# Performance work log

Hardware: AMD Instinct MI355X
Metric: run time of the kernel (lower is better)

The kernel has to match this reference:

```python
import jax, jax.numpy as jnp
import numpy as np

CH = 16        # channel_n
HID = 128      # hidden_size
IN_CH = 3      # input_channels (locked each step)
FIRE_RATE = 0.5


def _dwconv3x3(x, w, b):
    # depthwise 3x3, reflect padding (torch padding_mode='reflect', padding=1)
    xp = jnp.pad(x, ((0, 0), (0, 0), (1, 1), (1, 1)), mode='reflect')
    y = jax.lax.conv_general_dilated(
        xp, w, window_strides=(1, 1), padding='VALID',
        dimension_numbers=('NCHW', 'OIHW', 'NCHW'), feature_group_count=CH)
    return y + b[None, :, None, None]


def _conv1x1(x, w, b=None):
    # w: (out_ch, in_ch) -- squeezed 1x1 conv kernel
    y = jnp.einsum('bchw,oc->bohw', x, w)
    return y if b is None else y + b[None, :, None, None]


def setup_inputs() -> dict:
    key = jax.random.key(0)
    ks = jax.random.split(key, 8)
    B, H, W = 4, 256, 256
    x = jax.random.normal(ks[0], (B, CH, H, W), dtype=jnp.float32)
    # depthwise kernels: (CH, 1, 3, 3)
    p0_w = jax.random.normal(ks[1], (CH, 1, 3, 3), dtype=jnp.float32) * (1.0 / 3.0)
    p0_b = jax.random.normal(ks[2], (CH,), dtype=jnp.float32) * 0.1
    p1_w = jax.random.normal(ks[3], (CH, 1, 3, 3), dtype=jnp.float32) * (1.0 / 3.0)
    p1_b = jax.random.normal(ks[4], (CH,), dtype=jnp.float32) * 0.1
    # fc0: Conv2d(3*CH -> HID, k=1); fc1: Conv2d(HID -> CH, k=1, bias=False)
    fc0_w = jax.random.normal(ks[5], (HID, 3 * CH), dtype=jnp.float32) * (1.0 / np.sqrt(3 * CH))
    fc0_b = jax.random.normal(ks[6], (HID,), dtype=jnp.float32) * 0.1
    # NOTE: torch zero-inits fc1; we use small random weights so the reference is non-trivial.
    fc1_w = jax.random.normal(ks[7], (CH, HID), dtype=jnp.float32) * (0.1 / np.sqrt(HID))
    return {"x": x, "p0_w": p0_w, "p0_b": p0_b, "p1_w": p1_w, "p1_b": p1_b,
            "fc0_w": fc0_w, "fc0_b": fc0_b, "fc1_w": fc1_w, "steps": 32}


def reference(x, p0_w, p0_b, p1_w, p1_b, fc0_w, fc0_b, fc1_w, steps):
    B, _, H, W = x.shape
    input_image = x[:, :IN_CH]  # clone of input channels, re-written each step
    keys = jax.random.split(jax.random.key(42), steps)

    @jax.checkpoint
    def step(x, key):
        # perceive: depthwise 3x3 x2, concat with state
        z1 = _dwconv3x3(x, p0_w, p0_b)
        z2 = _dwconv3x3(x, p1_w, p1_b)
        y = jnp.concatenate([x, z1, z2], axis=1)        # [B, 3*CH, H, W]
        # 1x1-conv MLP
        dx = jax.nn.relu(_conv1x1(y, fc0_w, fc0_b))      # [B, HID, H, W]
        dx = _conv1x1(dx, fc1_w)                         # [B, CH, H, W]
        # stochastic fire mask: rand > fire_rate, broadcast over channels
        mask = (jax.random.uniform(key, (B, 1, H, W), dtype=x.dtype) > FIRE_RATE).astype(x.dtype)
        x = x + dx * mask                                # residual update
        x = x.at[:, :IN_CH].set(input_image)             # channel lock
        return x, None

    x, _ = jax.lax.scan(step, x, keys)
    out = x[:, 3]  # segmentation channel
    return out, x
```

## Files before the change

### kernel.cpp

```cpp
#include <hip/hip_runtime.h>
#include <cstdint>

#define CH     16
#define HPIX   256
#define WPIX   256
#define BATCH  4
#define HID    128
#define STEPS  32
#define PLANE  (HPIX * WPIX)
#define MASK_N (BATCH * PLANE)

#define TW 16
#define TH 8
#define XTW 18
#define XTH 10
#define NPX (XTH * XTW)
#define HSF 20

typedef _Float16 half8  __attribute__((ext_vector_type(8)));
typedef _Float16 half4e __attribute__((ext_vector_type(4)));
typedef float floatx4  __attribute__((ext_vector_type(4)));
typedef float floatx16 __attribute__((ext_vector_type(16)));

__host__ __device__ static inline void tf2x32(uint32_t k0, uint32_t k1,
                                              uint32_t x0, uint32_t x1,
                                              uint32_t& o0, uint32_t& o1) {
  const uint32_t ks2 = k0 ^ k1 ^ 0x1BD11BDAu;
#define TFROT(a) { x0 += x1; x1 = (x1 << (a)) | (x1 >> (32 - (a))); x1 ^= x0; }
  x0 += k0;  x1 += k1;
  TFROT(13) TFROT(15) TFROT(26) TFROT(6)
  x0 += k1;  x1 += ks2 + 1u;
  TFROT(17) TFROT(29) TFROT(16) TFROT(24)
  x0 += ks2; x1 += k0 + 2u;
  TFROT(13) TFROT(15) TFROT(26) TFROT(6)
  x0 += k0;  x1 += k1 + 3u;
  TFROT(17) TFROT(29) TFROT(16) TFROT(24)
  x0 += k1;  x1 += ks2 + 4u;
  TFROT(13) TFROT(15) TFROT(26) TFROT(6)
  x0 += ks2; x1 += k0 + 5u;
#undef TFROT
  o0 = x0; o1 = x1;
}

__global__ __launch_bounds__(256) void prep_weights(
    const float* __restrict__ fc0_w, const float* __restrict__ fc0_b,
    const float* __restrict__ fc1_w,
    const float* __restrict__ p0_w, const float* __restrict__ p0_b,
    const float* __restrict__ p1_w, const float* __restrict__ p1_b,
    _Float16* __restrict__ Mh, _Float16* __restrict__ W1h,
    float* __restrict__ bp) {
  const int idx = blockIdx.x * 256 + threadIdx.x;
  if (idx < 9 * HID * CH) {
    const int tap = idx / (HID * CH);
    const int rem = idx - tap * (HID * CH);
    const int h = rem >> 4, c = rem & 15;
    float m = fc0_w[h * 48 + 16 + c] * p0_w[c * 9 + tap]
            + fc0_w[h * 48 + 32 + c] * p1_w[c * 9 + tap];
    if (tap == 4) m += fc0_w[h * 48 + c];
    Mh[(tap * HID + h) * CH + c] = (_Float16)m;
  } else if (idx < 9 * HID * CH + CH * HID) {
    const int i2 = idx - 9 * HID * CH;
    W1h[i2] = (_Float16)fc1_w[i2];
  } else if (idx < 9 * HID * CH + CH * HID + HID) {
    const int h = idx - (9 * HID * CH + CH * HID);
    float s = fc0_b[h];
    for (int c = 0; c < CH; ++c)
      s += fc0_w[h * 48 + 16 + c] * p0_b[c]
         + fc0_w[h * 48 + 32 + c] * p1_b[c];
    bp[h] = s;
  }
}

__global__ __launch_bounds__(256) void nca_step(
    const float* __restrict__ x_in, float* __restrict__ x_out,
    const float* __restrict__ x0,
    const _Float16* __restrict__ Mh, const _Float16* __restrict__ W1h,
    const float* __restrict__ bp,
    uint32_t k0, uint32_t k1, int wrgb) {
  __shared__ __align__(16) _Float16 halo[NPX * HSF];
  __shared__ __align__(16) _Float16 Hbuf[64 * HID];
  __shared__ float maskbuf[128];

  const int tid = threadIdx.x;
  const int w0 = blockIdx.x * TW;
  const int h0 = blockIdx.y * TH;
  const int b  = blockIdx.z;

  const int wv   = tid >> 6;
  const int lane = tid & 63;
  const int n    = lane & 15;
  const int g    = lane >> 4;
  const int c32  = lane & 31;
  const int q2   = lane >> 5;

  const float* __restrict__ xb  = x_in + (size_t)b * CH * PLANE;
  const float* __restrict__ x0b = x0   + (size_t)b * CH * PLANE;

  half8 Atap[9];
  #pragma unroll
  for (int t = 0; t < 9; ++t)
    Atap[t] = *(const half8*)(Mh + ((t * HID + 32 * wv + c32) << 4) + 8 * q2);
  half8 bw1[4];
  #pragma unroll
  for (int s = 0; s < 4; ++s)
    bw1[s] = *(const half8*)(W1h + n * HID + 32 * s + 8 * g);
  float4 bias4[4];
  #pragma unroll
  for (int rb = 0; rb < 4; ++rb)
    bias4[rb] = *(const float4*)(bp + 32 * wv + 8 * rb + 4 * q2);

  float4 xcv[2];
  size_t xoff[2];
  #pragma unroll
  for (int i = 0; i < 2; ++i) {
    xoff[i] = (size_t)n * PLANE + (size_t)(h0 + 4 * i + wv) * WPIX + w0 + 4 * g;
    xcv[i] = *(const float4*)(((n < 3) ? x0b : xb) + xoff[i]);
  }

  if (tid < NPX) {
    const int hr = tid / XTW, hc = tid - (tid / XTW) * XTW;
    int gh = h0 + hr - 1;
    gh = (gh < 0) ? -gh : ((gh > HPIX - 1) ? (2 * (HPIX - 1) - gh) : gh);
    int gw = w0 + hc - 1;
    gw = (gw < 0) ? -gw : ((gw > WPIX - 1) ? (2 * (WPIX - 1) - gw) : gw);
    const float* __restrict__ srcS = xb  + gh * WPIX + gw;
    const float* __restrict__ src0 = x0b + gh * WPIX + gw;
    #pragma unroll
    for (int blk = 0; blk < 4; ++blk) {
      half4e h4;
      #pragma unroll
      for (int e = 0; e < 4; ++e) {
        const int c = 4 * blk + e;
        h4[e] = (_Float16)((c < 3 ? src0 : srcS)[(size_t)c * PLANE]);
      }
      *(half4e*)(halo + tid * HSF + 4 * blk) = h4;
    }
  }

  if (lane < 32) {
    const int pxl = wv * 32 + lane;
    const int hp = h0 + (pxl >> 4), wp = w0 + (pxl & 15);
    const uint32_t j = (uint32_t)(b * PLANE + hp * WPIX + wp);
    uint32_t r0, r1;
    tf2x32(k0, k1, 0u, j, r0, r1);
    const uint32_t bits = r0 ^ r1;
    union { uint32_t i; float f; } cvt;
    cvt.i = (bits >> 9) | 0x3F800000u;
    maskbuf[pxl] = ((cvt.f - 1.0f) > 0.5f) ? 1.0f : 0.0f;
  }
  __syncthreads();

  float* __restrict__ xob = x_out + (size_t)b * CH * PLANE;

  #pragma unroll
  for (int half = 0; half < 2; ++half) {
    #pragma unroll
    for (int cti = 0; cti < 2; ++cti) {
      const int ct   = 2 * half + cti;
      const int prow = 2 * ct + (c32 >> 4);
      const int pcol = c32 & 15;
      half8 btap[9];
      #pragma unroll
      for (int dr = 0; dr < 3; ++dr) {
        #pragma unroll
        for (int dj = 0; dj < 3; ++dj) {
          const _Float16* hp =
              halo + ((prow + dr) * XTW + pcol + dj) * HSF + 8 * q2;
          const half4e lo = *(const half4e*)hp;
          const half4e hi = *(const half4e*)(hp + 4);
          half8 ff;
          ff[0] = lo[0]; ff[1] = lo[1]; ff[2] = lo[2]; ff[3] = lo[3];
          ff[4] = hi[0]; ff[5] = hi[1]; ff[6] = hi[2]; ff[7] = hi[3];
          btap[dr * 3 + dj] = ff;
        }
      }
      floatx16 acc = {0.f,0.f,0.f,0.f,0.f,0.f,0.f,0.f,
                      0.f,0.f,0.f,0.f,0.f,0.f,0.f,0.f};
      #pragma unroll
      for (int t = 0; t < 9; ++t)
        acc = __builtin_amdgcn_mfma_f32_32x32x16_f16(Atap[t], btap[t], acc,
                                                     0, 0, 0);
      const int px  = 32 * ct + c32;
      const int ph  = px & 63;
      const int n16 = px & 15;
      #pragma unroll
      for (int rb = 0; rb < 4; ++rb) {
        half4e hv;
        hv[0] = (_Float16)fmaxf(acc[4 * rb + 0] + bias4[rb].x, 0.f);
        hv[1] = (_Float16)fmaxf(acc[4 * rb + 1] + bias4[rb].y, 0.f);
        hv[2] = (_Float16)fmaxf(acc[4 * rb + 2] + bias4[rb].z, 0.f);
        hv[3] = (_Float16)fmaxf(acc[4 * rb + 3] + bias4[rb].w, 0.f);
        *(half4e*)(Hbuf + ph * HID + (((4 * wv + rb) ^ n16) << 3) + 4 * q2) = hv;
      }
    }
    __syncthreads();

    {
      const int ct2 = 4 * half + wv;
      floatx4 c2 = {0.f, 0.f, 0.f, 0.f};
      #pragma unroll
      for (int ks = 0; ks < 4; ++ks) {
        const half8 a2 = *(const half8*)(
            Hbuf + (16 * (ct2 & 3) + n) * HID + (((4 * ks + g) ^ n) << 3));
        c2 = __builtin_amdgcn_mfma_f32_16x16x32_f16(a2, bw1[ks], c2, 0, 0, 0);
      }
      const float4 mk = *(const float4*)(maskbuf + 16 * ct2 + 4 * g);
      const float4 xc = xcv[half];
      float4 res;
      res.x = (n < 3) ? xc.x : fmaf(mk.x, c2[0], xc.x);
      res.y = (n < 3) ? xc.y : fmaf(mk.y, c2[1], xc.y);
      res.z = (n < 3) ? xc.z : fmaf(mk.z, c2[2], xc.z);
      res.w = (n < 3) ? xc.w : fmaf(mk.w, c2[3], xc.w);
      if (n >= 3 || wrgb)
        *(float4*)(xob + xoff[half]) = res;
    }
    if (half == 0) __syncthreads();
  }
}

__global__ __launch_bounds__(256) void extract_ch3(
    const float* __restrict__ xf, float* __restrict__ out) {
  const int i = blockIdx.x * 256 + threadIdx.x;
  if (i >= MASK_N) return;
  const int b = i >> 16;
  const int p = i & (PLANE - 1);
  out[i] = xf[((size_t)b * CH + 3) * PLANE + p];
}

extern "C" void kernel_launch(void* const* d_in, const int* in_sizes, int n_in,
                              void* d_out, int out_size, void* d_ws, size_t ws_size,
                              hipStream_t stream) {
  const float* x     = (const float*)d_in[0];
  const float* p0_w  = (const float*)d_in[1];
  const float* p0_b  = (const float*)d_in[2];
  const float* p1_w  = (const float*)d_in[3];
  const float* p1_b  = (const float*)d_in[4];
  const float* fc0_w = (const float*)d_in[5];
  const float* fc0_b = (const float*)d_in[6];
  const float* fc1_w = (const float*)d_in[7];

  uint32_t kk[STEPS][2];
  for (int i = 0; i < STEPS; ++i) {
    uint32_t a, b2;
    tf2x32(0u, 42u, 0u, (uint32_t)i, a, b2);
    kk[i][0] = a;
    kk[i][1] = b2;
  }

  float* out = (float*)d_out;
  _Float16* Mh  = (_Float16*)d_out;
  _Float16* W1h = Mh + 9 * HID * CH;
  float*    bpr = (float*)((char*)d_out + (9 * HID * CH + CH * HID) * 2);
  float* bufA = out + MASK_N;
  float* bufB = (float*)d_ws;

  const int prep_n = 9 * HID * CH + CH * HID + HID;
  prep_weights<<<dim3((prep_n + 255) / 256), dim3(256), 0, stream>>>(
      fc0_w, fc0_b, fc1_w, p0_w, p0_b, p1_w, p1_b, Mh, W1h, bpr);

  const dim3 grid(WPIX / TW, HPIX / TH, BATCH);
  const dim3 block(256);

  for (int i = 0; i < STEPS; ++i) {
    const float* src = (i == 0) ? x : ((i & 1) ? bufB : bufA);
    float* dst = (i & 1) ? bufA : bufB;
    nca_step<<<grid, block, 0, stream>>>(src, dst, x, Mh, W1h, bpr,
                                         kk[i][0], kk[i][1],
                                         (i == STEPS - 1) ? 1 : 0);
  }
  extract_ch3<<<dim3(MASK_N / 256), dim3(256), 0, stream>>>(bufA, out);
}
```

Measured before the change: 733.4 us.

## Process two batch images per block and fuse channel-3 extraction into last step

Each block now handles two batch images, halving the grid and amortising the per-block register loads of the MFMA weight fragments and biases over twice the work. The bias is folded into the accumulator initialisation, and the final step writes channel 3 directly to the output, removing the separate extract kernel. Prepared weights move from the output buffer to the workspace. The trade-off is more LDS per block (doubled halo and mask), fewer blocks for occupancy and latency hiding, and a longer serial phase loop with extra barriers.

```diff
diff --git a/kernel.cpp b/kernel.cpp
--- a/kernel.cpp
+++ b/kernel.cpp
@@ -75,16 +75,16 @@
     const float* __restrict__ x_in, float* __restrict__ x_out,
     const float* __restrict__ x0,
     const _Float16* __restrict__ Mh, const _Float16* __restrict__ W1h,
-    const float* __restrict__ bp,
-    uint32_t k0, uint32_t k1, int wrgb) {
-  __shared__ __align__(16) _Float16 halo[NPX * HSF];
+    const float* __restrict__ bp, float* __restrict__ outp,
+    uint32_t k0, uint32_t k1, int wfin) {
+  __shared__ __align__(16) _Float16 halo[2][NPX * HSF];
   __shared__ __align__(16) _Float16 Hbuf[64 * HID];
-  __shared__ float maskbuf[128];
+  __shared__ float maskbuf[2][128];
 
   const int tid = threadIdx.x;
   const int w0 = blockIdx.x * TW;
   const int h0 = blockIdx.y * TH;
-  const int b  = blockIdx.z;
+  const int bz = blockIdx.z;
 
   const int wv   = tid >> 6;
   const int lane = tid & 63;
@@ -93,9 +93,6 @@
   const int c32  = lane & 31;
   const int q2   = lane >> 5;
 
-  const float* __restrict__ xb  = x_in + (size_t)b * CH * PLANE;
-  const float* __restrict__ x0b = x0   + (size_t)b * CH * PLANE;
-
   half8 Atap[9];
   #pragma unroll
   for (int t = 0; t < 9; ++t)
@@ -109,22 +106,30 @@
   for (int rb = 0; rb < 4; ++rb)
     bias4[rb] = *(const float4*)(bp + 32 * wv + 8 * rb + 4 * q2);
 
-  float4 xcv[2];
-  size_t xoff[2];
-  #pragma unroll
-  for (int i = 0; i < 2; ++i) {
-    xoff[i] = (size_t)n * PLANE + (size_t)(h0 + 4 * i + wv) * WPIX + w0 + 4 * g;
-    xcv[i] = *(const float4*)(((n < 3) ? x0b : xb) + xoff[i]);
-  }
-
-  if (tid < NPX) {
-    const int hr = tid / XTW, hc = tid - (tid / XTW) * XTW;
+  float4 xcv[2][2];
+  #pragma unroll
+  for (int bt = 0; bt < 2; ++bt) {
+    const int b = 2 * bz + bt;
+    const float* __restrict__ base =
+        ((n < 3) ? x0 : x_in) + (size_t)b * CH * PLANE;
+    #pragma unroll
+    for (int hf = 0; hf < 2; ++hf)
+      xcv[bt][hf] = *(const float4*)(base + (size_t)n * PLANE +
+                                     (size_t)(h0 + 4 * hf + wv) * WPIX +
+                                     w0 + 4 * g);
+  }
+
+  for (int job = tid; job < 2 * NPX; job += 256) {
+    const int bt = (job >= NPX);
+    const int px = job - NPX * bt;
+    const int b  = 2 * bz + bt;
+    const int hr = px / XTW, hc = px - (px / XTW) * XTW;
     int gh = h0 + hr - 1;
     gh = (gh < 0) ? -gh : ((gh > HPIX - 1) ? (2 * (HPIX - 1) - gh) : gh);
     int gw = w0 + hc - 1;
     gw = (gw < 0) ? -gw : ((gw > WPIX - 1) ? (2 * (WPIX - 1) - gw) : gw);
-    const float* __restrict__ srcS = xb  + gh * WPIX + gw;
-    const float* __restrict__ src0 = x0b + gh * WPIX + gw;
+    const float* __restrict__ srcS = x_in + (size_t)b * CH * PLANE + gh * WPIX + gw;
+    const float* __restrict__ src0 = x0   + (size_t)b * CH * PLANE + gh * WPIX + gw;
     #pragma unroll
     for (int blk = 0; blk < 4; ++blk) {
       half4e h4;
@@ -133,12 +138,14 @@
         const int c = 4 * blk + e;
         h4[e] = (_Float16)((c < 3 ? src0 : srcS)[(size_t)c * PLANE]);
       }
-      *(half4e*)(halo + tid * HSF + 4 * blk) = h4;
+      *(half4e*)(&halo[bt][px * HSF + 4 * blk]) = h4;
     }
   }
 
-  if (lane < 32) {
-    const int pxl = wv * 32 + lane;
+  {
+    const int bt  = tid >> 7;
+    const int pxl = tid & 127;
+    const int b   = 2 * bz + bt;
     const int hp = h0 + (pxl >> 4), wp = w0 + (pxl & 15);
     const uint32_t j = (uint32_t)(b * PLANE + hp * WPIX + wp);
     uint32_t r0, r1;
@@ -146,17 +153,18 @@
     const uint32_t bits = r0 ^ r1;
     union { uint32_t i; float f; } cvt;
     cvt.i = (bits >> 9) | 0x3F800000u;
-    maskbuf[pxl] = ((cvt.f - 1.0f) > 0.5f) ? 1.0f : 0.0f;
+    maskbuf[bt][pxl] = ((cvt.f - 1.0f) > 0.5f) ? 1.0f : 0.0f;
   }
   __syncthreads();
 
-  float* __restrict__ xob = x_out + (size_t)b * CH * PLANE;
-
-  #pragma unroll
-  for (int half = 0; half < 2; ++half) {
+  #pragma unroll
+  for (int ph = 0; ph < 4; ++ph) {
+    const int bt = ph >> 1, hf = ph & 1;
+    const _Float16* __restrict__ hb = halo[bt];
+
     #pragma unroll
     for (int cti = 0; cti < 2; ++cti) {
-      const int ct   = 2 * half + cti;
+      const int ct   = 2 * hf + cti;
       const int prow = 2 * ct + (c32 >> 4);
       const int pcol = c32 & 15;
       half8 btap[9];
@@ -165,7 +173,7 @@
         #pragma unroll
         for (int dj = 0; dj < 3; ++dj) {
           const _Float16* hp =
-              halo + ((prow + dr) * XTW + pcol + dj) * HSF + 8 * q2;
+              hb + ((prow + dr) * XTW + pcol + dj) * HSF + 8 * q2;
           const half4e lo = *(const half4e*)hp;
           const half4e hi = *(const half4e*)(hp + 4);
           half8 ff;
@@ -174,29 +182,36 @@
           btap[dr * 3 + dj] = ff;
         }
       }
-      floatx16 acc = {0.f,0.f,0.f,0.f,0.f,0.f,0.f,0.f,
-                      0.f,0.f,0.f,0.f,0.f,0.f,0.f,0.f};
+      floatx16 acc;
+      #pragma unroll
+      for (int rb = 0; rb < 4; ++rb) {
+        acc[4 * rb + 0] = bias4[rb].x;
+        acc[4 * rb + 1] = bias4[rb].y;
+        acc[4 * rb + 2] = bias4[rb].z;
+        acc[4 * rb + 3] = bias4[rb].w;
+      }
       #pragma unroll
       for (int t = 0; t < 9; ++t)
         acc = __builtin_amdgcn_mfma_f32_32x32x16_f16(Atap[t], btap[t], acc,
                                                      0, 0, 0);
       const int px  = 32 * ct + c32;
-      const int ph  = px & 63;
+      const int phx = px & 63;
       const int n16 = px & 15;
       #pragma unroll
       for (int rb = 0; rb < 4; ++rb) {
         half4e hv;
-        hv[0] = (_Float16)fmaxf(acc[4 * rb + 0] + bias4[rb].x, 0.f);
-        hv[1] = (_Float16)fmaxf(acc[4 * rb + 1] + bias4[rb].y, 0.f);
-        hv[2] = (_Float16)fmaxf(acc[4 * rb + 2] + bias4[rb].z, 0.f);
-        hv[3] = (_Float16)fmaxf(acc[4 * rb + 3] + bias4[rb].w, 0.f);
-        *(half4e*)(Hbuf + ph * HID + (((4 * wv + rb) ^ n16) << 3) + 4 * q2) = hv;
+        hv[0] = (_Float16)fmaxf(acc[4 * rb + 0], 0.f);
+        hv[1] = (_Float16)fmaxf(acc[4 * rb + 1], 0.f);
+        hv[2] = (_Float16)fmaxf(acc[4 * rb + 2], 0.f);
+        hv[3] = (_Float16)fmaxf(acc[4 * rb + 3], 0.f);
+        *(half4e*)(Hbuf + phx * HID + (((4 * wv + rb) ^ n16) << 3) + 4 * q2) = hv;
       }
     }
     __syncthreads();
 
     {
-      const int ct2 = 4 * half + wv;
+      const int ct2 = 4 * hf + wv;
+      const int b   = 2 * bz + bt;
       floatx4 c2 = {0.f, 0.f, 0.f, 0.f};
       #pragma unroll
       for (int ks = 0; ks < 4; ++ks) {
@@ -204,27 +219,23 @@
             Hbuf + (16 * (ct2 & 3) + n) * HID + (((4 * ks + g) ^ n) << 3));
         c2 = __builtin_amdgcn_mfma_f32_16x16x32_f16(a2, bw1[ks], c2, 0, 0, 0);
       }
-      const float4 mk = *(const float4*)(maskbuf + 16 * ct2 + 4 * g);
-      const float4 xc = xcv[half];
+      const float4 mk = *(const float4*)(&maskbuf[bt][16 * ct2 + 4 * g]);
+      const float4 xc = xcv[bt][hf];
       float4 res;
       res.x = (n < 3) ? xc.x : fmaf(mk.x, c2[0], xc.x);
       res.y = (n < 3) ? xc.y : fmaf(mk.y, c2[1], xc.y);
       res.z = (n < 3) ? xc.z : fmaf(mk.z, c2[2], xc.z);
       res.w = (n < 3) ? xc.w : fmaf(mk.w, c2[3], xc.w);
-      if (n >= 3 || wrgb)
-        *(float4*)(xob + xoff[half]) = res;
+      const size_t off = (size_t)n * PLANE +
+                         (size_t)(h0 + ct2) * WPIX + w0 + 4 * g;
+      if (n >= 3 || wfin)
+        *(float4*)(x_out + (size_t)b * CH * PLANE + off) = res;
+      if (wfin && n == 3)
+        *(float4*)(outp + (size_t)b * PLANE +
+                   (size_t)(h0 + ct2) * WPIX + w0 + 4 * g) = res;
     }
-    if (half == 0) __syncthreads();
-  }
-}
-
-__global__ __launch_bounds__(256) void extract_ch3(
-    const float* __restrict__ xf, float* __restrict__ out) {
-  const int i = blockIdx.x * 256 + threadIdx.x;
-  if (i >= MASK_N) return;
-  const int b = i >> 16;
-  const int p = i & (PLANE - 1);
-  out[i] = xf[((size_t)b * CH + 3) * PLANE + p];
+    if (ph < 3) __syncthreads();
+  }
 }
 
 extern "C" void kernel_launch(void* const* d_in, const int* in_sizes, int n_in,
@@ -247,26 +258,25 @@
     kk[i][1] = b2;
   }
 
-  float* out = (float*)d_out;
-  _Float16* Mh  = (_Float16*)d_out;
-  _Float16* W1h = Mh + 9 * HID * CH;
-  float*    bpr = (float*)((char*)d_out + (9 * HID * CH + CH * HID) * 2);
+  float* out  = (float*)d_out;
   float* bufA = out + MASK_N;
   float* bufB = (float*)d_ws;
+  _Float16* Mh  = (_Float16*)((char*)d_ws + (size_t)(32 << 20));
+  _Float16* W1h = Mh + 9 * HID * CH;
+  float*    bpr = (float*)((char*)(W1h + CH * HID));
 
   const int prep_n = 9 * HID * CH + CH * HID + HID;
   prep_weights<<<dim3((prep_n + 255) / 256), dim3(256), 0, stream>>>(
       fc0_w, fc0_b, fc1_w, p0_w, p0_b, p1_w, p1_b, Mh, W1h, bpr);
 
-  const dim3 grid(WPIX / TW, HPIX / TH, BATCH);
+  const dim3 grid(WPIX / TW, HPIX / TH, BATCH / 2);
   const dim3 block(256);
 
   for (int i = 0; i < STEPS; ++i) {
     const float* src = (i == 0) ? x : ((i & 1) ? bufB : bufA);
     float* dst = (i & 1) ? bufA : bufB;
-    nca_step<<<grid, block, 0, stream>>>(src, dst, x, Mh, W1h, bpr,
+    nca_step<<<grid, block, 0, stream>>>(src, dst, x, Mh, W1h, bpr, out,
                                          kk[i][0], kk[i][1],
                                          (i == STEPS - 1) ? 1 : 0);
   }
-  extract_ch3<<<dim3(MASK_N / 256), dim3(256), 0, stream>>>(bufA, out);
-}
+}
```

Measured after the change: 766.7 us. +4.5%, slower.
